# Optimization experiments

Hardware: AMD Instinct MI355X
Metric: run time of the kernel (lower is better)

Reference implementation:

```python
import jax, jax.numpy as jnp
import numpy as np

N = 50000        # num_nodes
E = 1_600_000    # num_edges (before self loops)
IN = 128         # in_channels
C = 16           # out_channels per head
H = 4            # heads
ED = 16          # edge_dim
SLOPE = 0.2      # LeakyReLU negative slope


def setup_inputs() -> dict:
    key = jax.random.key(0)
    ks = jax.random.split(key, 9)
    x = jax.random.normal(ks[0], (N, IN), jnp.float32)
    edge_index = jax.random.randint(ks[1], (2, E), 0, N)
    edge_attr = jax.random.normal(ks[2], (E, ED), jnp.float32)
    # GATConv parameters (PyG layout): node lin (no bias), attention vectors, edge lin
    W = jax.random.normal(ks[3], (IN, H * C), jnp.float32) / np.float32(np.sqrt(IN))
    att_src = jax.random.normal(ks[4], (H, C), jnp.float32) / np.float32(np.sqrt(C))
    att_dst = jax.random.normal(ks[5], (H, C), jnp.float32) / np.float32(np.sqrt(C))
    W_edge = jax.random.normal(ks[6], (ED, H * C), jnp.float32) / np.float32(np.sqrt(ED))
    att_edge = jax.random.normal(ks[7], (H, C), jnp.float32) / np.float32(np.sqrt(C))
    bias = jnp.zeros((H * C,), jnp.float32)
    return {"x": x, "edge_index": edge_index, "edge_attr": edge_attr,
            "W": W, "att_src": att_src, "att_dst": att_dst,
            "W_edge": W_edge, "att_edge": att_edge, "bias": bias}


def reference(x, edge_index, edge_attr, W, att_src, att_dst, W_edge, att_edge, bias):
    num_nodes = x.shape[0]
    # GATLayer: add self loops (PyG fills self-loop edge_attr with 1.0)
    loops = jnp.arange(num_nodes, dtype=edge_index.dtype)
    ei = jnp.concatenate([edge_index, jnp.stack([loops, loops])], axis=1)
    ea = jnp.concatenate(
        [edge_attr, jnp.ones((num_nodes, edge_attr.shape[1]), edge_attr.dtype)], axis=0)
    src, dst = ei[0], ei[1]  # messages flow src -> dst
    # eval mode: feat_dropout / edge_dropout are no-ops
    h = (x @ W).reshape(num_nodes, H, C)              # [N,H,C]
    a_src = jnp.einsum('nhc,hc->nh', h, att_src)       # [N,H]
    a_dst = jnp.einsum('nhc,hc->nh', h, att_dst)       # [N,H]
    e = (ea @ W_edge).reshape(-1, H, C)                # [E',H,C]
    a_e = jnp.einsum('ehc,hc->eh', e, att_edge)        # [E',H]
    alpha = a_src[src] + a_dst[dst] + a_e              # per-edge logits [E',H]
    alpha = jax.nn.leaky_relu(alpha, SLOPE)
    # segment softmax over incoming edges of each dst node (every node has a self loop)
    amax = jax.ops.segment_max(alpha, dst, num_segments=num_nodes)
    ex = jnp.exp(alpha - amax[dst])
    denom = jax.ops.segment_sum(ex, dst, num_segments=num_nodes)
    att = ex / denom[dst]                              # [E',H]
    # scatter-add aggregation of weighted source features
    out = jax.ops.segment_sum(att[:, :, None] * h[src], dst, num_segments=num_nodes)
    return out.reshape(num_nodes, H * C) + bias        # concat heads + bias
```

## Files before the change

kernel.cpp:

```cpp
#include <hip/hip_runtime.h>
#include <hip/hip_bf16.h>
#include <cstdint>

#define IN_CH 128
#define HC    64
#define ED    16
#define SLOPE 0.2f

__device__ __forceinline__ uint32_t f2bf(float x) {
  uint32_t b = __float_as_uint(x);
  return (b + 0x7fffu + ((b >> 16) & 1u)) >> 16;
}
__device__ __forceinline__ float bf2f(uint32_t h) {
  return __uint_as_float(h << 16);
}

__global__ __launch_bounds__(256) void k_node(
    const float* __restrict__ x, const float* __restrict__ W,
    const float* __restrict__ att_src_p, const float* __restrict__ att_dst_p,
    float* __restrict__ h, float* __restrict__ a_src, float* __restrict__ a_dst,
    int N)
{
  int lane = threadIdx.x & 63;
  int gw = (blockIdx.x * blockDim.x + threadIdx.x) >> 6;
  int nwaves = (gridDim.x * blockDim.x) >> 6;
  float asv = att_src_p[lane];
  float adv = att_dst_p[lane];
  for (int n0 = gw * 4; n0 < N; n0 += nwaves * 4) {
    int n1 = min(n0 + 1, N - 1), n2 = min(n0 + 2, N - 1), n3 = min(n0 + 3, N - 1);
    const float4* xa = (const float4*)(x + (size_t)n0 * IN_CH);
    const float4* xb = (const float4*)(x + (size_t)n1 * IN_CH);
    const float4* xc = (const float4*)(x + (size_t)n2 * IN_CH);
    const float4* xd = (const float4*)(x + (size_t)n3 * IN_CH);
    float acc0 = 0.f, acc1 = 0.f, acc2 = 0.f, acc3 = 0.f;
#pragma unroll 4
    for (int k4 = 0; k4 < IN_CH / 4; k4++) {
      float4 va = xa[k4], vb = xb[k4], vc = xc[k4], vd = xd[k4];
      float w0 = W[(k4 * 4 + 0) * HC + lane];
      float w1 = W[(k4 * 4 + 1) * HC + lane];
      float w2 = W[(k4 * 4 + 2) * HC + lane];
      float w3 = W[(k4 * 4 + 3) * HC + lane];
      acc0 += va.x * w0 + va.y * w1 + va.z * w2 + va.w * w3;
      acc1 += vb.x * w0 + vb.y * w1 + vb.z * w2 + vb.w * w3;
      acc2 += vc.x * w0 + vc.y * w1 + vc.z * w2 + vc.w * w3;
      acc3 += vd.x * w0 + vd.y * w1 + vd.z * w2 + vd.w * w3;
    }
    h[(size_t)n0 * HC + lane] = acc0;
    if (n0 + 1 < N) h[(size_t)n1 * HC + lane] = acc1;
    if (n0 + 2 < N) h[(size_t)n2 * HC + lane] = acc2;
    if (n0 + 3 < N) h[(size_t)n3 * HC + lane] = acc3;
    float s0 = acc0 * asv, s1 = acc1 * asv, s2 = acc2 * asv, s3 = acc3 * asv;
    float d0 = acc0 * adv, d1 = acc1 * adv, d2 = acc2 * adv, d3 = acc3 * adv;
#pragma unroll
    for (int m = 1; m < 16; m <<= 1) {
      s0 += __shfl_xor(s0, m); s1 += __shfl_xor(s1, m);
      s2 += __shfl_xor(s2, m); s3 += __shfl_xor(s3, m);
      d0 += __shfl_xor(d0, m); d1 += __shfl_xor(d1, m);
      d2 += __shfl_xor(d2, m); d3 += __shfl_xor(d3, m);
    }
    if ((lane & 15) == 0) {
      int hh = lane >> 4;
      a_src[(size_t)n0 * 4 + hh] = s0; a_dst[(size_t)n0 * 4 + hh] = d0;
      if (n0 + 1 < N) { a_src[(size_t)n1 * 4 + hh] = s1; a_dst[(size_t)n1 * 4 + hh] = d1; }
      if (n0 + 2 < N) { a_src[(size_t)n2 * 4 + hh] = s2; a_dst[(size_t)n2 * 4 + hh] = d2; }
      if (n0 + 3 < N) { a_src[(size_t)n3 * 4 + hh] = s3; a_dst[(size_t)n3 * 4 + hh] = d3; }
    }
  }
}

__global__ __launch_bounds__(256) void k_hist(const int* __restrict__ dst, int E,
                                              int* __restrict__ deg)
{
  int e = blockIdx.x * 256 + threadIdx.x;
  if (e < E) atomicAdd(&deg[dst[e]], 1);
}

__global__ __launch_bounds__(256) void k_scan_a(const int* __restrict__ deg, int N,
                                                int* __restrict__ rowptr,
                                                int* __restrict__ blksums)
{
  __shared__ int tsum[256];
  int tid = threadIdx.x;
  int base = blockIdx.x * 2048 + tid * 8;
  int pre[8];
  int s = 0;
#pragma unroll
  for (int j = 0; j < 8; j++) {
    int idx = base + j;
    int v = (idx < N) ? deg[idx] : 0;
    pre[j] = s; s += v;
  }
  tsum[tid] = s;
  __syncthreads();
  for (int offm = 1; offm < 256; offm <<= 1) {
    int t = (tid >= offm) ? tsum[tid - offm] : 0;
    __syncthreads();
    tsum[tid] += t;
    __syncthreads();
  }
  int excl = tsum[tid] - s;
#pragma unroll
  for (int j = 0; j < 8; j++) {
    int idx = base + j;
    if (idx < N) rowptr[idx] = excl + pre[j];
  }
  if (tid == 255) blksums[blockIdx.x] = tsum[255];
}

__global__ void k_scan_b(int* __restrict__ blksums, int NB)
{
  if (threadIdx.x == 0 && blockIdx.x == 0) {
    int run = 0;
    for (int b = 0; b < NB; b++) { int t = blksums[b]; blksums[b] = run; run += t; }
  }
}

__global__ __launch_bounds__(256) void k_scan_c(int* __restrict__ rowptr,
                                                const int* __restrict__ blksums,
                                                int N, int E)
{
  int i = blockIdx.x * 256 + threadIdx.x;
  if (i < N) rowptr[i] += blksums[i >> 11];
  if (i == 0) rowptr[N] = E;
}

__global__ __launch_bounds__(256) void k_edge3(
    const int* __restrict__ ei, const float* __restrict__ ea,
    const float* __restrict__ W_edge, const float* __restrict__ att_edge,
    const float* __restrict__ a_src, const float* __restrict__ a_dst,
    const int* __restrict__ rowptr, int* __restrict__ cursor,
    uint4* __restrict__ pay, int E)
{
  __shared__ float ve[ED * 4];
  if (threadIdx.x < 64) {
    int d = threadIdx.x >> 2, hh = threadIdx.x & 3;
    float s = 0.f;
#pragma unroll
    for (int c = 0; c < 16; c++) s += W_edge[d * HC + hh * 16 + c] * att_edge[hh * 16 + c];
    ve[d * 4 + hh] = s;
  }
  __syncthreads();
  int e = blockIdx.x * 256 + threadIdx.x;
  if (e >= E) return;
  int sn = ei[e], dn = ei[E + e];
  float4 as4 = *(const float4*)(a_src + (size_t)sn * 4);
  float4 ad4 = *(const float4*)(a_dst + (size_t)dn * 4);
  const float4* ea4 = (const float4*)(ea + (size_t)e * ED);
  float4 q0 = ea4[0], q1 = ea4[1], q2 = ea4[2], q3 = ea4[3];
  float eav[16] = {q0.x,q0.y,q0.z,q0.w, q1.x,q1.y,q1.z,q1.w,
                   q2.x,q2.y,q2.z,q2.w, q3.x,q3.y,q3.z,q3.w};
  float ae0 = 0.f, ae1 = 0.f, ae2 = 0.f, ae3 = 0.f;
#pragma unroll
  for (int d = 0; d < ED; d++) {
    float v = eav[d];
    ae0 += v * ve[d * 4 + 0]; ae1 += v * ve[d * 4 + 1];
    ae2 += v * ve[d * 4 + 2]; ae3 += v * ve[d * 4 + 3];
  }
  float al0 = as4.x + ad4.x + ae0;
  float al1 = as4.y + ad4.y + ae1;
  float al2 = as4.z + ad4.z + ae2;
  float al3 = as4.w + ad4.w + ae3;
  al0 = al0 > 0.f ? al0 : SLOPE * al0;
  al1 = al1 > 0.f ? al1 : SLOPE * al1;
  al2 = al2 > 0.f ? al2 : SLOPE * al2;
  al3 = al3 > 0.f ? al3 : SLOPE * al3;
  int pos = rowptr[dn] + atomicAdd(&cursor[dn], 1);
  uint4 r;
  r.x = (uint32_t)sn;
  r.y = f2bf(__expf(al0)) | (f2bf(__expf(al1)) << 16);
  r.z = f2bf(__expf(al2)) | (f2bf(__expf(al3)) << 16);
  r.w = 0u;
  pay[pos] = r;
}

__global__ __launch_bounds__(256) void k_agg3(
    const float* __restrict__ h,
    const float* __restrict__ a_src, const float* __restrict__ a_dst,
    const float* __restrict__ W_edge, const float* __restrict__ att_edge,
    const float* __restrict__ bias, const int* __restrict__ rowptr,
    const uint4* __restrict__ pay, float* __restrict__ out, int N)
{
  __shared__ float aes[4];
  if (threadIdx.x < 4) {
    int hh = threadIdx.x;
    float s = 0.f;
    for (int d = 0; d < ED; d++) {
      float vd = 0.f;
#pragma unroll
      for (int c = 0; c < 16; c++) vd += W_edge[d * HC + hh * 16 + c] * att_edge[hh * 16 + c];
      s += vd;
    }
    aes[hh] = s;
  }
  __syncthreads();
  int lane = threadIdx.x & 63;
  int n = blockIdx.x * 4 + (threadIdx.x >> 6);
  if (n >= N) return;
  int hq = lane >> 4;
  int b = rowptr[n], e = rowptr[n + 1];
  float acc = 0.f, den = 0.f;
  int p = b;
  for (; p + 3 < e; p += 4) {
    uint4 r0 = pay[p], r1 = pay[p + 1], r2 = pay[p + 2], r3 = pay[p + 3];
    uint32_t w0 = (hq & 2) ? r0.z : r0.y;
    uint32_t w1 = (hq & 2) ? r1.z : r1.y;
    uint32_t w2 = (hq & 2) ? r2.z : r2.y;
    uint32_t w3 = (hq & 2) ? r3.z : r3.y;
    float e0 = bf2f((hq & 1) ? (w0 >> 16) : (w0 & 0xffffu));
    float e1 = bf2f((hq & 1) ? (w1 >> 16) : (w1 & 0xffffu));
    float e2 = bf2f((hq & 1) ? (w2 >> 16) : (w2 & 0xffffu));
    float e3 = bf2f((hq & 1) ? (w3 >> 16) : (w3 & 0xffffu));
    float h0 = h[(size_t)r0.x * HC + lane];
    float h1 = h[(size_t)r1.x * HC + lane];
    float h2 = h[(size_t)r2.x * HC + lane];
    float h3 = h[(size_t)r3.x * HC + lane];
    acc += e0 * h0 + e1 * h1 + e2 * h2 + e3 * h3;
    den += (e0 + e1) + (e2 + e3);
  }
  for (; p < e; p++) {
    uint4 r0 = pay[p];
    uint32_t w0 = (hq & 2) ? r0.z : r0.y;
    float e0 = bf2f((hq & 1) ? (w0 >> 16) : (w0 & 0xffffu));
    acc += e0 * h[(size_t)r0.x * HC + lane];
    den += e0;
  }
  float al = a_src[(size_t)n * 4 + hq] + a_dst[(size_t)n * 4 + hq] + aes[hq];
  al = al > 0.f ? al : SLOPE * al;
  float exs = __expf(al);
  acc += exs * h[(size_t)n * HC + lane];
  den += exs;
  out[(size_t)n * HC + lane] = acc / den + bias[lane];
}

extern "C" void kernel_launch(void* const* d_in, const int* in_sizes, int n_in,
                              void* d_out, int out_size, void* d_ws, size_t ws_size,
                              hipStream_t stream)
{
  const float* x        = (const float*)d_in[0];
  const int*   ei       = (const int*)d_in[1];
  const float* ea       = (const float*)d_in[2];
  const float* W        = (const float*)d_in[3];
  const float* att_src  = (const float*)d_in[4];
  const float* att_dst  = (const float*)d_in[5];
  const float* W_edge   = (const float*)d_in[6];
  const float* att_edge = (const float*)d_in[7];
  const float* bias     = (const float*)d_in[8];
  float* out = (float*)d_out;

  int N = in_sizes[0] / IN_CH;
  int E = in_sizes[1] / 2;

  uint8_t* ws = (uint8_t*)d_ws;
  size_t off = 0;
  auto alloc = [&](size_t bytes) -> void* {
    void* p = ws + off;
    off = (off + bytes + 255) & ~(size_t)255;
    return p;
  };
  float* h        = (float*)alloc((size_t)N * HC * 4);
  float* a_src_w  = (float*)alloc((size_t)N * 4 * 4);
  float* a_dst_w  = (float*)alloc((size_t)N * 4 * 4);
  int*   deg      = (int*)alloc((size_t)N * 2 * 4);
  int*   cursor   = deg + N;
  int*   rowptr   = (int*)alloc(((size_t)N + 1) * 4);
  int*   blksums  = (int*)alloc(64 * 4);
  uint4* pay      = (uint4*)alloc((size_t)E * 16);
  (void)ws_size; (void)n_in; (void)out_size;

  hipMemsetAsync(deg, 0, (size_t)N * 2 * 4, stream);

  k_node<<<512, 256, 0, stream>>>(x, W, att_src, att_dst, h, a_src_w, a_dst_w, N);
  k_hist<<<(E + 255) / 256, 256, 0, stream>>>(ei + E, E, deg);
  int NB = (N + 2047) / 2048;
  k_scan_a<<<NB, 256, 0, stream>>>(deg, N, rowptr, blksums);
  k_scan_b<<<1, 64, 0, stream>>>(blksums, NB);
  k_scan_c<<<(N + 255) / 256, 256, 0, stream>>>(rowptr, blksums, N, E);
  k_edge3<<<(E + 255) / 256, 256, 0, stream>>>(ei, ea, W_edge, att_edge,
                                               a_src_w, a_dst_w, rowptr, cursor,
                                               pay, E);
  k_agg3<<<(N + 3) / 4, 256, 0, stream>>>(h, a_src_w, a_dst_w, W_edge, att_edge,
                                          bias, rowptr, pay, out, N);
}
```

Baseline: 506.6 us.

## Replace per-node CSR sort with 128-node bucket partition and shared-memory atomic aggregation

Swaps the per-destination-node histogram, three-stage scan and global per-node atomic scatter for a coarse bucketing of edges into 128-node buckets. Edges are locally counted in shared memory per 4096-edge chunk, reserved in bulk with one global atomic per bucket, and aggregation accumulates per-bucket into shared-memory accumulators using LDS float atomics. This removes most global atomics and scan kernels, but adds LDS atomic contention in the aggregation and a 32KB+ shared accumulator per block. With 391 buckets, aggregation parallelism drops to about 391 blocks.

```diff
diff --git a/kernel.cpp b/kernel.cpp
--- a/kernel.cpp
+++ b/kernel.cpp
@@ -6,6 +6,11 @@
 #define HC    64
 #define ED    16
 #define SLOPE 0.2f
+
+#define BK      128
+#define BKSH    7
+#define NBMAX   512
+#define CHUNK   4096
 
 __device__ __forceinline__ uint32_t f2bf(float x) {
   uint32_t b = __float_as_uint(x);
@@ -68,121 +73,130 @@
   }
 }
 
-__global__ __launch_bounds__(256) void k_hist(const int* __restrict__ dst, int E,
-                                              int* __restrict__ deg)
-{
-  int e = blockIdx.x * 256 + threadIdx.x;
-  if (e < E) atomicAdd(&deg[dst[e]], 1);
-}
-
-__global__ __launch_bounds__(256) void k_scan_a(const int* __restrict__ deg, int N,
-                                                int* __restrict__ rowptr,
-                                                int* __restrict__ blksums)
-{
-  __shared__ int tsum[256];
+__global__ __launch_bounds__(256) void k_bhist(const int* __restrict__ dst, int E,
+                                               int* __restrict__ bdeg, int NB)
+{
+  __shared__ int c[NBMAX];
+  for (int i = threadIdx.x; i < NBMAX; i += 256) c[i] = 0;
+  __syncthreads();
+  for (int e = blockIdx.x * 256 + threadIdx.x; e < E; e += gridDim.x * 256)
+    atomicAdd(&c[dst[e] >> BKSH], 1);
+  __syncthreads();
+  for (int b = threadIdx.x; b < NB; b += 256) {
+    int v = c[b];
+    if (v) atomicAdd(&bdeg[b], v);
+  }
+}
+
+__global__ __launch_bounds__(NBMAX) void k_bscan(const int* __restrict__ bdeg, int NB,
+                                                 int* __restrict__ bbase,
+                                                 int* __restrict__ bcursor)
+{
+  __shared__ int s[NBMAX];
   int tid = threadIdx.x;
-  int base = blockIdx.x * 2048 + tid * 8;
-  int pre[8];
-  int s = 0;
-#pragma unroll
-  for (int j = 0; j < 8; j++) {
-    int idx = base + j;
-    int v = (idx < N) ? deg[idx] : 0;
-    pre[j] = s; s += v;
-  }
-  tsum[tid] = s;
-  __syncthreads();
-  for (int offm = 1; offm < 256; offm <<= 1) {
-    int t = (tid >= offm) ? tsum[tid - offm] : 0;
+  int v = (tid < NB) ? bdeg[tid] : 0;
+  s[tid] = v;
+  __syncthreads();
+  for (int o = 1; o < NBMAX; o <<= 1) {
+    int t = (tid >= o) ? s[tid - o] : 0;
     __syncthreads();
-    tsum[tid] += t;
+    s[tid] += t;
     __syncthreads();
   }
-  int excl = tsum[tid] - s;
-#pragma unroll
-  for (int j = 0; j < 8; j++) {
-    int idx = base + j;
-    if (idx < N) rowptr[idx] = excl + pre[j];
-  }
-  if (tid == 255) blksums[blockIdx.x] = tsum[255];
-}
-
-__global__ void k_scan_b(int* __restrict__ blksums, int NB)
-{
-  if (threadIdx.x == 0 && blockIdx.x == 0) {
-    int run = 0;
-    for (int b = 0; b < NB; b++) { int t = blksums[b]; blksums[b] = run; run += t; }
-  }
-}
-
-__global__ __launch_bounds__(256) void k_scan_c(int* __restrict__ rowptr,
-                                                const int* __restrict__ blksums,
-                                                int N, int E)
-{
-  int i = blockIdx.x * 256 + threadIdx.x;
-  if (i < N) rowptr[i] += blksums[i >> 11];
-  if (i == 0) rowptr[N] = E;
-}
-
-__global__ __launch_bounds__(256) void k_edge3(
+  if (tid < NB) {
+    bbase[tid + 1] = s[tid];
+    bcursor[tid]   = s[tid] - v;
+    if (tid == 0) bbase[0] = 0;
+  }
+}
+
+__global__ __launch_bounds__(512) void k_edgeB(
     const int* __restrict__ ei, const float* __restrict__ ea,
     const float* __restrict__ W_edge, const float* __restrict__ att_edge,
     const float* __restrict__ a_src, const float* __restrict__ a_dst,
-    const int* __restrict__ rowptr, int* __restrict__ cursor,
-    uint4* __restrict__ pay, int E)
+    int* __restrict__ bcursor, uint4* __restrict__ tmp, int E, int NB)
 {
   __shared__ float ve[ED * 4];
-  if (threadIdx.x < 64) {
-    int d = threadIdx.x >> 2, hh = threadIdx.x & 3;
+  __shared__ int cnt[NBMAX];
+  __shared__ int sbase[NBMAX];
+  int tid = threadIdx.x;
+  if (tid < 64) {
+    int d = tid >> 2, hh = tid & 3;
     float s = 0.f;
 #pragma unroll
     for (int c = 0; c < 16; c++) s += W_edge[d * HC + hh * 16 + c] * att_edge[hh * 16 + c];
     ve[d * 4 + hh] = s;
   }
-  __syncthreads();
-  int e = blockIdx.x * 256 + threadIdx.x;
-  if (e >= E) return;
-  int sn = ei[e], dn = ei[E + e];
-  float4 as4 = *(const float4*)(a_src + (size_t)sn * 4);
-  float4 ad4 = *(const float4*)(a_dst + (size_t)dn * 4);
-  const float4* ea4 = (const float4*)(ea + (size_t)e * ED);
-  float4 q0 = ea4[0], q1 = ea4[1], q2 = ea4[2], q3 = ea4[3];
-  float eav[16] = {q0.x,q0.y,q0.z,q0.w, q1.x,q1.y,q1.z,q1.w,
-                   q2.x,q2.y,q2.z,q2.w, q3.x,q3.y,q3.z,q3.w};
-  float ae0 = 0.f, ae1 = 0.f, ae2 = 0.f, ae3 = 0.f;
-#pragma unroll
-  for (int d = 0; d < ED; d++) {
-    float v = eav[d];
-    ae0 += v * ve[d * 4 + 0]; ae1 += v * ve[d * 4 + 1];
-    ae2 += v * ve[d * 4 + 2]; ae3 += v * ve[d * 4 + 3];
-  }
-  float al0 = as4.x + ad4.x + ae0;
-  float al1 = as4.y + ad4.y + ae1;
-  float al2 = as4.z + ad4.z + ae2;
-  float al3 = as4.w + ad4.w + ae3;
-  al0 = al0 > 0.f ? al0 : SLOPE * al0;
-  al1 = al1 > 0.f ? al1 : SLOPE * al1;
-  al2 = al2 > 0.f ? al2 : SLOPE * al2;
-  al3 = al3 > 0.f ? al3 : SLOPE * al3;
-  int pos = rowptr[dn] + atomicAdd(&cursor[dn], 1);
-  uint4 r;
-  r.x = (uint32_t)sn;
-  r.y = f2bf(__expf(al0)) | (f2bf(__expf(al1)) << 16);
-  r.z = f2bf(__expf(al2)) | (f2bf(__expf(al3)) << 16);
-  r.w = 0u;
-  pay[pos] = r;
-}
-
-__global__ __launch_bounds__(256) void k_agg3(
+  for (int i = tid; i < NBMAX; i += 512) cnt[i] = 0;
+  __syncthreads();
+
+  uint4 pl[CHUNK / 512];
+  int rk[CHUNK / 512];
+  int e0 = blockIdx.x * CHUNK + tid;
+#pragma unroll
+  for (int j = 0; j < CHUNK / 512; j++) {
+    int e = e0 + j * 512;
+    rk[j] = -1;
+    if (e < E) {
+      int sn = ei[e], dn = ei[E + e];
+      float4 as4 = *(const float4*)(a_src + (size_t)sn * 4);
+      float4 ad4 = *(const float4*)(a_dst + (size_t)dn * 4);
+      const float4* ea4 = (const float4*)(ea + (size_t)e * ED);
+      float4 q0 = ea4[0], q1 = ea4[1], q2 = ea4[2], q3 = ea4[3];
+      float eav[16] = {q0.x,q0.y,q0.z,q0.w, q1.x,q1.y,q1.z,q1.w,
+                       q2.x,q2.y,q2.z,q2.w, q3.x,q3.y,q3.z,q3.w};
+      float ae0 = 0.f, ae1 = 0.f, ae2 = 0.f, ae3 = 0.f;
+#pragma unroll
+      for (int d = 0; d < ED; d++) {
+        float v = eav[d];
+        ae0 += v * ve[d * 4 + 0]; ae1 += v * ve[d * 4 + 1];
+        ae2 += v * ve[d * 4 + 2]; ae3 += v * ve[d * 4 + 3];
+      }
+      float al0 = as4.x + ad4.x + ae0;
+      float al1 = as4.y + ad4.y + ae1;
+      float al2 = as4.z + ad4.z + ae2;
+      float al3 = as4.w + ad4.w + ae3;
+      al0 = al0 > 0.f ? al0 : SLOPE * al0;
+      al1 = al1 > 0.f ? al1 : SLOPE * al1;
+      al2 = al2 > 0.f ? al2 : SLOPE * al2;
+      al3 = al3 > 0.f ? al3 : SLOPE * al3;
+      uint4 r;
+      r.x = (uint32_t)sn;
+      r.y = f2bf(__expf(al0)) | (f2bf(__expf(al1)) << 16);
+      r.z = f2bf(__expf(al2)) | (f2bf(__expf(al3)) << 16);
+      r.w = (uint32_t)dn;
+      pl[j] = r;
+      rk[j] = atomicAdd(&cnt[dn >> BKSH], 1);
+    }
+  }
+  __syncthreads();
+  if (tid < NB) {
+    int c = cnt[tid];
+    if (c) sbase[tid] = atomicAdd(&bcursor[tid], c);
+  }
+  __syncthreads();
+#pragma unroll
+  for (int j = 0; j < CHUNK / 512; j++) {
+    if (rk[j] >= 0) {
+      int b = pl[j].w >> BKSH;
+      tmp[(size_t)sbase[b] + rk[j]] = pl[j];
+    }
+  }
+}
+
+__global__ __launch_bounds__(512) void k_aggB(
     const float* __restrict__ h,
     const float* __restrict__ a_src, const float* __restrict__ a_dst,
     const float* __restrict__ W_edge, const float* __restrict__ att_edge,
-    const float* __restrict__ bias, const int* __restrict__ rowptr,
-    const uint4* __restrict__ pay, float* __restrict__ out, int N)
-{
+    const float* __restrict__ bias, const int* __restrict__ bbase,
+    const uint4* __restrict__ tmp, float* __restrict__ out, int N)
+{
+  __shared__ float acc[BK * HC];
+  __shared__ float den[BK * 4];
   __shared__ float aes[4];
-  if (threadIdx.x < 4) {
-    int hh = threadIdx.x;
+  int tid = threadIdx.x;
+  if (tid < 4) {
+    int hh = tid;
     float s = 0.f;
     for (int d = 0; d < ED; d++) {
       float vd = 0.f;
@@ -192,16 +206,19 @@
     }
     aes[hh] = s;
   }
-  __syncthreads();
-  int lane = threadIdx.x & 63;
-  int n = blockIdx.x * 4 + (threadIdx.x >> 6);
-  if (n >= N) return;
-  int hq = lane >> 4;
-  int b = rowptr[n], e = rowptr[n + 1];
-  float acc = 0.f, den = 0.f;
-  int p = b;
-  for (; p + 3 < e; p += 4) {
-    uint4 r0 = pay[p], r1 = pay[p + 1], r2 = pay[p + 2], r3 = pay[p + 3];
+  for (int i = tid; i < BK * HC; i += 512) acc[i] = 0.f;
+  if (tid < BK * 4) den[tid] = 0.f;
+  __syncthreads();
+
+  int b = blockIdx.x;
+  int start = bbase[b], end = bbase[b + 1];
+  int cnt = end - start;
+  int lane = tid & 63, wv = tid >> 6, hq = lane >> 4;
+
+  int i = wv;
+  for (; i + 24 < cnt; i += 32) {
+    uint4 r0 = tmp[start + i],      r1 = tmp[start + i + 8];
+    uint4 r2 = tmp[start + i + 16], r3 = tmp[start + i + 24];
     uint32_t w0 = (hq & 2) ? r0.z : r0.y;
     uint32_t w1 = (hq & 2) ? r1.z : r1.y;
     uint32_t w2 = (hq & 2) ? r2.z : r2.y;
@@ -214,22 +231,38 @@
     float h1 = h[(size_t)r1.x * HC + lane];
     float h2 = h[(size_t)r2.x * HC + lane];
     float h3 = h[(size_t)r3.x * HC + lane];
-    acc += e0 * h0 + e1 * h1 + e2 * h2 + e3 * h3;
-    den += (e0 + e1) + (e2 + e3);
-  }
-  for (; p < e; p++) {
-    uint4 r0 = pay[p];
+    atomicAdd(&acc[(r0.w & (BK - 1)) * HC + lane], e0 * h0);
+    atomicAdd(&acc[(r1.w & (BK - 1)) * HC + lane], e1 * h1);
+    atomicAdd(&acc[(r2.w & (BK - 1)) * HC + lane], e2 * h2);
+    atomicAdd(&acc[(r3.w & (BK - 1)) * HC + lane], e3 * h3);
+    if ((lane & 15) == 0) {
+      atomicAdd(&den[(r0.w & (BK - 1)) * 4 + hq], e0);
+      atomicAdd(&den[(r1.w & (BK - 1)) * 4 + hq], e1);
+      atomicAdd(&den[(r2.w & (BK - 1)) * 4 + hq], e2);
+      atomicAdd(&den[(r3.w & (BK - 1)) * 4 + hq], e3);
+    }
+  }
+  for (; i < cnt; i += 8) {
+    uint4 r0 = tmp[start + i];
     uint32_t w0 = (hq & 2) ? r0.z : r0.y;
     float e0 = bf2f((hq & 1) ? (w0 >> 16) : (w0 & 0xffffu));
-    acc += e0 * h[(size_t)r0.x * HC + lane];
-    den += e0;
-  }
-  float al = a_src[(size_t)n * 4 + hq] + a_dst[(size_t)n * 4 + hq] + aes[hq];
-  al = al > 0.f ? al : SLOPE * al;
-  float exs = __expf(al);
-  acc += exs * h[(size_t)n * HC + lane];
-  den += exs;
-  out[(size_t)n * HC + lane] = acc / den + bias[lane];
+    float h0 = h[(size_t)r0.x * HC + lane];
+    atomicAdd(&acc[(r0.w & (BK - 1)) * HC + lane], e0 * h0);
+    if ((lane & 15) == 0) atomicAdd(&den[(r0.w & (BK - 1)) * 4 + hq], e0);
+  }
+  __syncthreads();
+
+  int n0 = b << BKSH;
+  for (int nL = wv; nL < BK; nL += 8) {
+    int n = n0 + nL;
+    if (n >= N) break;
+    float al = a_src[(size_t)n * 4 + hq] + a_dst[(size_t)n * 4 + hq] + aes[hq];
+    al = al > 0.f ? al : SLOPE * al;
+    float ex = __expf(al);
+    float o = (acc[nL * HC + lane] + ex * h[(size_t)n * HC + lane])
+            / (den[nL * 4 + hq] + ex) + bias[lane];
+    out[(size_t)n * HC + lane] = o;
+  }
 }
 
 extern "C" void kernel_launch(void* const* d_in, const int* in_sizes, int n_in,
@@ -249,6 +282,7 @@
 
   int N = in_sizes[0] / IN_CH;
   int E = in_sizes[1] / 2;
+  int NB = (N + BK - 1) / BK;
 
   uint8_t* ws = (uint8_t*)d_ws;
   size_t off = 0;
@@ -260,24 +294,20 @@
   float* h        = (float*)alloc((size_t)N * HC * 4);
   float* a_src_w  = (float*)alloc((size_t)N * 4 * 4);
   float* a_dst_w  = (float*)alloc((size_t)N * 4 * 4);
-  int*   deg      = (int*)alloc((size_t)N * 2 * 4);
-  int*   cursor   = deg + N;
-  int*   rowptr   = (int*)alloc(((size_t)N + 1) * 4);
-  int*   blksums  = (int*)alloc(64 * 4);
-  uint4* pay      = (uint4*)alloc((size_t)E * 16);
+  int*   bdeg     = (int*)alloc((size_t)NB * 4);
+  int*   bbase    = (int*)alloc(((size_t)NB + 1) * 4);
+  int*   bcursor  = (int*)alloc((size_t)NB * 4);
+  uint4* tmp      = (uint4*)alloc((size_t)E * 16);
   (void)ws_size; (void)n_in; (void)out_size;
 
-  hipMemsetAsync(deg, 0, (size_t)N * 2 * 4, stream);
+  hipMemsetAsync(bdeg, 0, (size_t)NB * 4, stream);
 
   k_node<<<512, 256, 0, stream>>>(x, W, att_src, att_dst, h, a_src_w, a_dst_w, N);
-  k_hist<<<(E + 255) / 256, 256, 0, stream>>>(ei + E, E, deg);
-  int NB = (N + 2047) / 2048;
-  k_scan_a<<<NB, 256, 0, stream>>>(deg, N, rowptr, blksums);
-  k_scan_b<<<1, 64, 0, stream>>>(blksums, NB);
-  k_scan_c<<<(N + 255) / 256, 256, 0, stream>>>(rowptr, blksums, N, E);
-  k_edge3<<<(E + 255) / 256, 256, 0, stream>>>(ei, ea, W_edge, att_edge,
-                                               a_src_w, a_dst_w, rowptr, cursor,
-                                               pay, E);
-  k_agg3<<<(N + 3) / 4, 256, 0, stream>>>(h, a_src_w, a_dst_w, W_edge, att_edge,
-                                          bias, rowptr, pay, out, N);
-}
+  k_bhist<<<512, 256, 0, stream>>>(ei + E, E, bdeg, NB);
+  k_bscan<<<1, NBMAX, 0, stream>>>(bdeg, NB, bbase, bcursor);
+  int nch = (E + CHUNK - 1) / CHUNK;
+  k_edgeB<<<nch, 512, 0, stream>>>(ei, ea, W_edge, att_edge,
+                                   a_src_w, a_dst_w, bcursor, tmp, E, NB);
+  k_aggB<<<NB, 512, 0, stream>>>(h, a_src_w, a_dst_w, W_edge, att_edge,
+                                 bias, bbase, tmp, out, N);
+}
```

New measurement: 1.042 ms. +105.7%, slower.

## Two-pass bucketed scatter of edge payloads into CSR order

Applied to the files above, without the earlier changes.

Replaces the single random scatter of per-edge payloads with two passes. First, each block computes attention logits for a 4096-edge chunk, groups the edges into coarse 128-node destination buckets using shared-memory counters, and writes them contiguously into a temp buffer. A second kernel, with an XCD-aware block swizzle, then places each edge at its exact CSR position. This aims to turn scattered global writes into more local ones, at the cost of an extra 16-byte-per-edge read/write pass, another temp buffer, and two extra launches.

```diff
diff --git a/kernel.cpp b/kernel.cpp
--- a/kernel.cpp
+++ b/kernel.cpp
@@ -6,6 +6,11 @@
 #define HC    64
 #define ED    16
 #define SLOPE 0.2f
+
+#define BK      128
+#define BKSH    7
+#define NBMAX   512
+#define CHUNK   4096
 
 __device__ __forceinline__ uint32_t f2bf(float x) {
   uint32_t b = __float_as_uint(x);
@@ -124,53 +129,103 @@
   if (i == 0) rowptr[N] = E;
 }
 
-__global__ __launch_bounds__(256) void k_edge3(
+__global__ __launch_bounds__(NBMAX) void k_binit(const int* __restrict__ rowptr,
+                                                 int* __restrict__ bcursor, int NB)
+{
+  int b = threadIdx.x;
+  if (b < NB) bcursor[b] = rowptr[b << BKSH];
+}
+
+__global__ __launch_bounds__(512) void k_edgeB(
     const int* __restrict__ ei, const float* __restrict__ ea,
     const float* __restrict__ W_edge, const float* __restrict__ att_edge,
     const float* __restrict__ a_src, const float* __restrict__ a_dst,
-    const int* __restrict__ rowptr, int* __restrict__ cursor,
-    uint4* __restrict__ pay, int E)
+    int* __restrict__ bcursor, uint4* __restrict__ tmp, int E, int NB)
 {
   __shared__ float ve[ED * 4];
-  if (threadIdx.x < 64) {
-    int d = threadIdx.x >> 2, hh = threadIdx.x & 3;
+  __shared__ int cnt[NBMAX];
+  __shared__ int sbase[NBMAX];
+  int tid = threadIdx.x;
+  if (tid < 64) {
+    int d = tid >> 2, hh = tid & 3;
     float s = 0.f;
 #pragma unroll
     for (int c = 0; c < 16; c++) s += W_edge[d * HC + hh * 16 + c] * att_edge[hh * 16 + c];
     ve[d * 4 + hh] = s;
   }
-  __syncthreads();
-  int e = blockIdx.x * 256 + threadIdx.x;
+  for (int i = tid; i < NBMAX; i += 512) cnt[i] = 0;
+  __syncthreads();
+
+  uint4 pl[CHUNK / 512];
+  int rk[CHUNK / 512];
+  int e0 = blockIdx.x * CHUNK + tid;
+#pragma unroll
+  for (int j = 0; j < CHUNK / 512; j++) {
+    int e = e0 + j * 512;
+    rk[j] = -1;
+    if (e < E) {
+      int sn = ei[e], dn = ei[E + e];
+      float4 as4 = *(const float4*)(a_src + (size_t)sn * 4);
+      float4 ad4 = *(const float4*)(a_dst + (size_t)dn * 4);
+      const float4* ea4 = (const float4*)(ea + (size_t)e * ED);
+      float4 q0 = ea4[0], q1 = ea4[1], q2 = ea4[2], q3 = ea4[3];
+      float eav[16] = {q0.x,q0.y,q0.z,q0.w, q1.x,q1.y,q1.z,q1.w,
+                       q2.x,q2.y,q2.z,q2.w, q3.x,q3.y,q3.z,q3.w};
+      float ae0 = 0.f, ae1 = 0.f, ae2 = 0.f, ae3 = 0.f;
+#pragma unroll
+      for (int d = 0; d < ED; d++) {
+        float v = eav[d];
+        ae0 += v * ve[d * 4 + 0]; ae1 += v * ve[d * 4 + 1];
+        ae2 += v * ve[d * 4 + 2]; ae3 += v * ve[d * 4 + 3];
+      }
+      float al0 = as4.x + ad4.x + ae0;
+      float al1 = as4.y + ad4.y + ae1;
+      float al2 = as4.z + ad4.z + ae2;
+      float al3 = as4.w + ad4.w + ae3;
+      al0 = al0 > 0.f ? al0 : SLOPE * al0;
+      al1 = al1 > 0.f ? al1 : SLOPE * al1;
+      al2 = al2 > 0.f ? al2 : SLOPE * al2;
+      al3 = al3 > 0.f ? al3 : SLOPE * al3;
+      uint4 r;
+      r.x = (uint32_t)sn;
+      r.y = f2bf(__expf(al0)) | (f2bf(__expf(al1)) << 16);
+      r.z = f2bf(__expf(al2)) | (f2bf(__expf(al3)) << 16);
+      r.w = (uint32_t)dn;
+      pl[j] = r;
+      rk[j] = atomicAdd(&cnt[dn >> BKSH], 1);
+    }
+  }
+  __syncthreads();
+  if (tid < NB) {
+    int c = cnt[tid];
+    if (c) sbase[tid] = atomicAdd(&bcursor[tid], c);
+  }
+  __syncthreads();
+#pragma unroll
+  for (int j = 0; j < CHUNK / 512; j++) {
+    if (rk[j] >= 0) {
+      int b = pl[j].w >> BKSH;
+      tmp[(size_t)sbase[b] + rk[j]] = pl[j];
+    }
+  }
+}
+
+__global__ __launch_bounds__(256) void k_place(
+    const uint4* __restrict__ tmp, const int* __restrict__ rowptr,
+    int* __restrict__ cursor, uint4* __restrict__ pay, int E)
+{
+  int nwg = gridDim.x;
+  int q = nwg >> 3, r = nwg & 7;
+  int bid = blockIdx.x;
+  int xcd = bid & 7, local = bid >> 3;
+  int swz = (xcd < r) ? xcd * (q + 1) + local
+                      : r * (q + 1) + (xcd - r) * q + local;
+  int e = swz * 256 + threadIdx.x;
   if (e >= E) return;
-  int sn = ei[e], dn = ei[E + e];
-  float4 as4 = *(const float4*)(a_src + (size_t)sn * 4);
-  float4 ad4 = *(const float4*)(a_dst + (size_t)dn * 4);
-  const float4* ea4 = (const float4*)(ea + (size_t)e * ED);
-  float4 q0 = ea4[0], q1 = ea4[1], q2 = ea4[2], q3 = ea4[3];
-  float eav[16] = {q0.x,q0.y,q0.z,q0.w, q1.x,q1.y,q1.z,q1.w,
-                   q2.x,q2.y,q2.z,q2.w, q3.x,q3.y,q3.z,q3.w};
-  float ae0 = 0.f, ae1 = 0.f, ae2 = 0.f, ae3 = 0.f;
-#pragma unroll
-  for (int d = 0; d < ED; d++) {
-    float v = eav[d];
-    ae0 += v * ve[d * 4 + 0]; ae1 += v * ve[d * 4 + 1];
-    ae2 += v * ve[d * 4 + 2]; ae3 += v * ve[d * 4 + 3];
-  }
-  float al0 = as4.x + ad4.x + ae0;
-  float al1 = as4.y + ad4.y + ae1;
-  float al2 = as4.z + ad4.z + ae2;
-  float al3 = as4.w + ad4.w + ae3;
-  al0 = al0 > 0.f ? al0 : SLOPE * al0;
-  al1 = al1 > 0.f ? al1 : SLOPE * al1;
-  al2 = al2 > 0.f ? al2 : SLOPE * al2;
-  al3 = al3 > 0.f ? al3 : SLOPE * al3;
+  uint4 t = tmp[e];
+  int dn = (int)t.w;
   int pos = rowptr[dn] + atomicAdd(&cursor[dn], 1);
-  uint4 r;
-  r.x = (uint32_t)sn;
-  r.y = f2bf(__expf(al0)) | (f2bf(__expf(al1)) << 16);
-  r.z = f2bf(__expf(al2)) | (f2bf(__expf(al3)) << 16);
-  r.w = 0u;
-  pay[pos] = r;
+  pay[pos] = t;
 }
 
 __global__ __launch_bounds__(256) void k_agg3(
@@ -249,6 +304,7 @@
 
   int N = in_sizes[0] / IN_CH;
   int E = in_sizes[1] / 2;
+  int NB = (N + BK - 1) / BK;
 
   uint8_t* ws = (uint8_t*)d_ws;
   size_t off = 0;
@@ -264,6 +320,8 @@
   int*   cursor   = deg + N;
   int*   rowptr   = (int*)alloc(((size_t)N + 1) * 4);
   int*   blksums  = (int*)alloc(64 * 4);
+  int*   bcursor  = (int*)alloc((size_t)NBMAX * 4);
+  uint4* tmp      = (uint4*)alloc((size_t)E * 16);
   uint4* pay      = (uint4*)alloc((size_t)E * 16);
   (void)ws_size; (void)n_in; (void)out_size;
 
@@ -271,13 +329,15 @@
 
   k_node<<<512, 256, 0, stream>>>(x, W, att_src, att_dst, h, a_src_w, a_dst_w, N);
   k_hist<<<(E + 255) / 256, 256, 0, stream>>>(ei + E, E, deg);
-  int NB = (N + 2047) / 2048;
-  k_scan_a<<<NB, 256, 0, stream>>>(deg, N, rowptr, blksums);
-  k_scan_b<<<1, 64, 0, stream>>>(blksums, NB);
+  int NBs = (N + 2047) / 2048;
+  k_scan_a<<<NBs, 256, 0, stream>>>(deg, N, rowptr, blksums);
+  k_scan_b<<<1, 64, 0, stream>>>(blksums, NBs);
   k_scan_c<<<(N + 255) / 256, 256, 0, stream>>>(rowptr, blksums, N, E);
-  k_edge3<<<(E + 255) / 256, 256, 0, stream>>>(ei, ea, W_edge, att_edge,
-                                               a_src_w, a_dst_w, rowptr, cursor,
-                                               pay, E);
+  k_binit<<<1, NBMAX, 0, stream>>>(rowptr, bcursor, NB);
+  int nch = (E + CHUNK - 1) / CHUNK;
+  k_edgeB<<<nch, 512, 0, stream>>>(ei, ea, W_edge, att_edge,
+                                   a_src_w, a_dst_w, bcursor, tmp, E, NB);
+  k_place<<<(E + 255) / 256, 256, 0, stream>>>(tmp, rowptr, cursor, pay, E);
   k_agg3<<<(N + 3) / 4, 256, 0, stream>>>(h, a_src_w, a_dst_w, W_edge, att_edge,
                                           bias, rowptr, pay, out, N);
 }
```

New measurement: 532.5 us. 5.1% more time.
